# Kernel tuning notes

Measured on AMD Instinct MI355X. Metric: run time of the kernel, lower is better.

The kernel has to match this reference:

```python
import jax, jax.numpy as jnp
import numpy as np

# quantization / activation scales (stand-ins for act_scales dict entries)
S_IN = 0.05      # in_proj:input
S_Z = 0.02       # in_proj:output (also gate/z scale)
S_U = 0.01       # x_proj:input (conv output scale)
S_DTLN = 0.02    # dt_layernorm:output
S_B = 0.02       # B_layernorm:output
S_C = 0.02       # C_layernorm:output
S_DT = 0.01      # dt_proj:output
S_Y = 0.01       # out_proj:input
EPS = 1e-6
R = 128          # time_step_rank
N = 16           # ssm_state_size


def qa(x, s):
    # simulate int8 activation quantization (values kept in fp32)
    return jnp.clip(jnp.round(x / s), -128.0, 127.0)


def qw(w):
    # per-tensor symmetric int8 weight quantization
    s = jnp.max(jnp.abs(w)) / 127.0
    return jnp.clip(jnp.round(w / s), -128.0, 127.0), s


def rmsnorm_q(x, w, s):
    x = x.astype(jnp.float32)
    x = x * jax.lax.rsqrt(jnp.mean(x * x, axis=-1, keepdims=True) + EPS)
    return qa(w * x, s)


def ssm_scan(u, dt, A, Bm, Cm):
    # u, dt: [B, D, S]; Bm, Cm: [B, S, N]; A: [D, N]
    def step(h, xs):
        dt_t, u_t, B_t, C_t = xs                     # [B,D],[B,D],[B,N],[B,N]
        dA = jnp.exp(dt_t[..., None] * A)            # [B,D,N]
        h = h * dA + (dt_t * u_t)[..., None] * B_t[:, None, :]
        y = jnp.einsum('bdn,bn->bd', h, C_t)
        return h, y
    Bsz, Dd, S = u.shape
    h0 = jnp.zeros((Bsz, Dd, A.shape[1]), u.dtype)
    xs = (jnp.moveaxis(dt, 2, 0), jnp.moveaxis(u, 2, 0),
          jnp.moveaxis(Bm, 1, 0), jnp.moveaxis(Cm, 1, 0))
    _, ys = jax.lax.scan(step, h0, xs)               # ys: [S,B,D]
    return jnp.moveaxis(ys, 0, 2)                    # [B,D,S]


def setup_inputs() -> dict:
    key = jax.random.key(0)
    ks = jax.random.split(key, 10)
    B, S, H, Din, K = 2, 2048, 2048, 4096, 4
    return {
        'hidden_states': jax.random.normal(ks[0], (B, S, H), jnp.float32),
        'in_proj_w': jax.random.normal(ks[1], (2 * Din, H), jnp.float32) * 0.02,
        'conv_w': jax.random.normal(ks[2], (Din, K), jnp.float32) * 0.1,
        'conv_b': jax.random.normal(ks[3], (Din,), jnp.float32) * 0.01,
        'x_proj_w': jax.random.normal(ks[4], (R + 2 * N, Din), jnp.float32) * 0.02,
        'dt_ln_w': jnp.ones((R,), jnp.float32),
        'B_ln_w': jnp.ones((N,), jnp.float32),
        'C_ln_w': jnp.ones((N,), jnp.float32),
        'dt_proj_w': jax.random.normal(ks[5], (Din, R), jnp.float32) * 0.05,
        'dt_bias': jax.random.normal(ks[6], (Din,), jnp.float32) * 0.5 - 4.0,
        'A_log': jnp.log(jnp.broadcast_to(jnp.arange(1, N + 1, dtype=jnp.float32), (Din, N))),
        'D_skip': jnp.ones((Din,), jnp.float32),
        'out_proj_w': jax.random.normal(ks[7], (H, Din), jnp.float32) * 0.02,
    }


def reference(hidden_states, in_proj_w, conv_w, conv_b, x_proj_w, dt_ln_w,
              B_ln_w, C_ln_w, dt_proj_w, dt_bias, A_log, D_skip, out_proj_w):
    # --- in_proj (W8A8B8O8), then seqlen-last layout [B, 2D, S] ---
    x_q = qa(hidden_states, S_IN)
    wq, ws = qw(in_proj_w)
    proj_q = qa((x_q @ wq.T) * (S_IN * ws), S_Z)          # [B,S,2D] int8-valued
    proj_q = jnp.swapaxes(proj_q, 1, 2)                   # [B,2D,S]
    Din = proj_q.shape[1] // 2
    hs_q, gate_q = proj_q[:, :Din], proj_q[:, Din:]

    # --- quantized causal depthwise conv1d + silu (QCausalConv1D) ---
    cwq, cws = qw(conv_w)
    K = conv_w.shape[1]
    conv_out = jax.lax.conv_general_dilated(
        hs_q, cwq[:, None, :], (1,), [(K - 1, 0)],
        dimension_numbers=('NCH', 'OIH', 'NCH'), feature_group_count=Din)
    conv_out = conv_out * (S_Z * cws) + conv_b[None, :, None]
    u_q = qa(jax.nn.silu(conv_out), S_U)                  # [B,Din,S]

    # --- x_proj (W8A8BF16OF16) -> dt/B/C, inner RMSNorms + quant ---
    xwq, xws = qw(x_proj_w)
    ssm_p = (jnp.swapaxes(u_q, 1, 2) @ xwq.T) * (S_U * xws)   # [B,S,R+2N] float
    dt_q = rmsnorm_q(ssm_p[..., :R], dt_ln_w, S_DTLN)
    B_q = rmsnorm_q(ssm_p[..., R:R + N], B_ln_w, S_B)
    C_q = rmsnorm_q(ssm_p[..., R + N:], C_ln_w, S_C)

    # --- dt_proj (W8A8B8O8, bias folded into scan) ---
    dwq, dws = qw(dt_proj_w)
    dt8 = qa((dt_q @ dwq.T) * (S_DTLN * dws), S_DT)       # [B,S,Din]
    dt = jax.nn.softplus(jnp.swapaxes(dt8, 1, 2) * S_DT + dt_bias[None, :, None])

    # --- selective scan (QSScan): dequantize, recur, gate ---
    u = u_q * S_U
    A = -jnp.exp(A_log)
    ys = ssm_scan(u, dt, A, B_q * S_B, C_q * S_C)         # [B,Din,S]
    ys = ys + u * D_skip[None, :, None]
    ys = ys * jax.nn.silu(gate_q * S_Z)

    # --- QAct + out_proj (W8A8BF16OF16) ---
    y_q = qa(jnp.swapaxes(ys, 1, 2), S_Y)                 # [B,S,Din]
    owq, ows = qw(out_proj_w)
    return (y_q @ owq.T) * (S_Y * ows)                    # [B,S,H]
```

## Files before the change

### kernel.cpp

```cpp
#include <hip/hip_runtime.h>
#include <stdint.h>

typedef signed char i8;
typedef int v4i __attribute__((ext_vector_type(4)));

#define S_IN  0.05f
#define S_Z   0.02f
#define S_U   0.01f
#define S_DTLN 0.02f
#define S_B   0.02f
#define S_C   0.02f
#define S_DT  0.01f
#define S_Y   0.01f

__device__ __forceinline__ float q8f(float x, float s) {
    float r = rintf(x / s);
    return fmaxf(-128.0f, fminf(127.0f, r));
}
__device__ __forceinline__ int q8i(float x, float s) { return (int)q8f(x, s); }

__device__ __forceinline__ float softplus_f(float x) {
    return __fadd_rn(fmaxf(x, 0.0f), log1pf(expf(-fabsf(x))));
}

__device__ __forceinline__ int sbyte_of(int w, int j) {
    return (int)(signed char)((unsigned)w >> (j * 8));
}
__device__ __forceinline__ int ubyte_of(int w, int j) {
    return (int)(((unsigned)w >> (j * 8)) & 255u);
}

__device__ __forceinline__ void gload16(const i8* g, i8* lds) {
    __builtin_amdgcn_global_load_lds(
        (const __attribute__((address_space(1))) unsigned int*)g,
        (__attribute__((address_space(3))) unsigned int*)lds,
        16, 0, 0);
}

__global__ __launch_bounds__(256)
void k_maxabs(const float* __restrict__ w, long long n, unsigned* __restrict__ out) {
    unsigned m = 0;
    long long stride = (long long)gridDim.x * 256;
    for (long long i = (long long)blockIdx.x * 256 + threadIdx.x; i < n; i += stride)
        m = max(m, __float_as_uint(fabsf(w[i])));
    #pragma unroll
    for (int off = 32; off; off >>= 1) {
        unsigned o = (unsigned)__shfl_xor((int)m, off);
        m = max(m, o);
    }
    __shared__ unsigned sm[4];
    if ((threadIdx.x & 63) == 0) sm[threadIdx.x >> 6] = m;
    __syncthreads();
    if (threadIdx.x == 0) {
        unsigned r = max(max(sm[0], sm[1]), max(sm[2], sm[3]));
        atomicMax(out, r);
    }
}

__global__ __launch_bounds__(256)
void k_quant_w(const float* __restrict__ w, long long n,
               const unsigned* __restrict__ maxbits, i8* __restrict__ o) {
    long long i = ((long long)blockIdx.x * 256 + threadIdx.x) * 4;
    if (i >= n) return;
    float s = __uint_as_float(*maxbits) / 127.0f;
    float4 v = *(const float4*)(w + i);
    unsigned pk = ((unsigned)(q8i(v.x, s) & 255))
                | ((unsigned)(q8i(v.y, s) & 255) << 8)
                | ((unsigned)(q8i(v.z, s) & 255) << 16)
                | ((unsigned)(q8i(v.w, s) & 255) << 24);
    *(unsigned*)(o + i) = pk;
}

__global__ __launch_bounds__(256)
void k_quant_x(const float* __restrict__ x, long long n, float s, i8* __restrict__ o) {
    long long i = ((long long)blockIdx.x * 256 + threadIdx.x) * 4;
    if (i >= n) return;
    float4 v = *(const float4*)(x + i);
    unsigned pk = ((unsigned)(q8i(v.x, s) & 255))
                | ((unsigned)(q8i(v.y, s) & 255) << 8)
                | ((unsigned)(q8i(v.z, s) & 255) << 16)
                | ((unsigned)(q8i(v.w, s) & 255) << 24);
    *(unsigned*)(o + i) = pk;
}

template<int EPI>
__global__ __launch_bounds__(256)
void k_mgemm(const i8* __restrict__ A, const i8* __restrict__ Bw,
             int M, int N, int K,
             const unsigned* __restrict__ wmaxbits,
             void* __restrict__ out0, void* __restrict__ out1) {
    __shared__ i8 sA[16384];
    __shared__ i8 sB[16384];
    const int tid = threadIdx.x;
    const int w = tid >> 6;
    const int l = tid & 63;
    int id = blockIdx.y * gridDim.x + blockIdx.x;
    const int qq = (gridDim.x * gridDim.y) >> 3;
    id = (id & 7) * qq + (id >> 3);
    const int m0 = (id / gridDim.x) << 7;
    const int n0 = (id % gridDim.x) << 7;
    const int lr = l & 15;
    const int lk = l >> 4;
    const i8* gA = A  + (size_t)(m0 + lr) * K + lk * 16;
    const i8* gB = Bw + (size_t)(n0 + lr) * K + lk * 16;
    const size_t rowK16 = (size_t)16 * K;
    const int mw = (w >> 1) * 4;
    const int nw = (w & 1) * 4;
    const int rdoff = lk * 256 + lr * 16;
    v4i acc[4][4] = {};
    for (int k0 = 0; k0 < K; k0 += 128) {
        gload16(gA + rowK16 * w + k0,            sA + w * 2048);
        gload16(gA + rowK16 * w + k0 + 64,       sA + w * 2048 + 1024);
        gload16(gA + rowK16 * (4 + w) + k0,      sA + (4 + w) * 2048);
        gload16(gA + rowK16 * (4 + w) + k0 + 64, sA + (4 + w) * 2048 + 1024);
        gload16(gB + rowK16 * w + k0,            sB + w * 2048);
        gload16(gB + rowK16 * w + k0 + 64,       sB + w * 2048 + 1024);
        gload16(gB + rowK16 * (4 + w) + k0,      sB + (4 + w) * 2048);
        gload16(gB + rowK16 * (4 + w) + k0 + 64, sB + (4 + w) * 2048 + 1024);
        __syncthreads();
        #pragma unroll
        for (int k64 = 0; k64 < 2; k64++) {
            v4i af[4], bf[4];
            #pragma unroll
            for (int t = 0; t < 4; t++) {
                af[t] = *(const v4i*)(sA + (mw + t) * 2048 + k64 * 1024 + rdoff);
                bf[t] = *(const v4i*)(sB + (nw + t) * 2048 + k64 * 1024 + rdoff);
            }
            #pragma unroll
            for (int mt = 0; mt < 4; mt++)
                #pragma unroll
                for (int nt = 0; nt < 4; nt++)
                    acc[mt][nt] = __builtin_amdgcn_mfma_i32_16x16x64_i8(af[mt], bf[nt], acc[mt][nt], 0, 0, 0);
        }
        __syncthreads();
    }
    const float wsc = __uint_as_float(*wmaxbits) / 127.0f;
    const int m0w = m0 + (w >> 1) * 64;
    const int n0w = n0 + (w & 1) * 64;
    if constexpr (EPI == 0 || EPI == 2) {
        const float sc = (EPI == 0 ? S_IN : S_DTLN) * wsc;
        const float qs = (EPI == 0 ? S_Z : S_DT);
        const int b = m0w >> 11;
        #pragma unroll
        for (int nt = 0; nt < 4; nt++) {
            const int j = n0w + nt * 16 + lr;
            i8* dst;
            if constexpr (EPI == 0) dst = (j < 4096) ? (i8*)out0 : (i8*)out1;
            else dst = (i8*)out0;
            const int jj = j & 4095;
            #pragma unroll
            for (int mt = 0; mt < 4; mt++) {
                const int sbase = (m0w & 2047) + mt * 16 + lk * 4;
                unsigned pk = 0;
                #pragma unroll
                for (int r = 0; r < 4; r++) {
                    float v = (float)acc[mt][nt][r] * sc;
                    pk |= ((unsigned)(q8i(v, qs) & 255)) << (8 * r);
                }
                *(unsigned*)(dst + ((size_t)b * 4096 + jj) * 2048 + sbase) = pk;
            }
        }
    } else if constexpr (EPI == 1) {
        const float sc = S_U * wsc;
        float* O = (float*)out0;
        #pragma unroll
        for (int mt = 0; mt < 4; mt++)
            #pragma unroll
            for (int r = 0; r < 4; r++) {
                const int m = m0w + mt * 16 + lk * 4 + r;
                #pragma unroll
                for (int nt = 0; nt < 4; nt++) {
                    const int j = n0w + nt * 16 + lr;
                    if (j < 160)
                        O[(size_t)m * 160 + j] = (float)acc[mt][nt][r] * sc;
                }
            }
    } else {
        const float sc = S_Y * wsc;
        float* O = (float*)out0;
        #pragma unroll
        for (int mt = 0; mt < 4; mt++)
            #pragma unroll
            for (int r = 0; r < 4; r++) {
                const int m = m0w + mt * 16 + lk * 4 + r;
                #pragma unroll
                for (int nt = 0; nt < 4; nt++)
                    O[(size_t)m * N + n0w + nt * 16 + lr] = (float)acc[mt][nt][r] * sc;
            }
    }
}

__global__ __launch_bounds__(256)
void k_conv(const i8* __restrict__ hsq, const i8* __restrict__ cwq,
            const float* __restrict__ conv_b, const unsigned* __restrict__ cmaxbits,
            i8* __restrict__ uq, i8* __restrict__ uqT) {
    __shared__ char lt[64][68];
    const int tid = threadIdx.x;
    const int b = blockIdx.z;
    const int d0 = blockIdx.y << 6;
    const int s0 = blockIdx.x << 6;
    const int dl = tid >> 2;
    const int sg = tid & 3;
    const int d = d0 + dl;
    const int sbase = s0 + (sg << 4);
    const i8* xp = hsq + ((size_t)b * 4096 + d) * 2048;
    int v[19];
    #pragma unroll
    for (int i = 0; i < 19; i++) {
        int s = sbase - 3 + i;
        v[i] = (s >= 0) ? (int)xp[s] : 0;
    }
    const unsigned cw = *(const unsigned*)(cwq + (size_t)d * 4);
    const int w0 = (int)(char)(cw & 255);
    const int w1 = (int)(char)((cw >> 8) & 255);
    const int w2 = (int)(char)((cw >> 16) & 255);
    const int w3 = (int)(char)((cw >> 24) & 255);
    const float cws = __uint_as_float(*cmaxbits) / 127.0f;
    const float sc = S_Z * cws;
    const float bias = conv_b[d];
    unsigned pk[4] = {0, 0, 0, 0};
    #pragma unroll
    for (int t = 0; t < 16; t++) {
        int acc = v[t] * w0 + v[t + 1] * w1 + v[t + 2] * w2 + v[t + 3] * w3;
        float f = __fadd_rn(__fmul_rn((float)acc, sc), bias);
        float sig = 1.0f / (1.0f + expf(-f));
        float sl = __fmul_rn(f, sig);
        int q = q8i(sl, S_U);
        pk[t >> 2] |= ((unsigned)(q & 255)) << ((t & 3) * 8);
        lt[(sg << 4) + t][dl] = (char)q;
    }
    *(int4*)(uq + ((size_t)b * 4096 + d) * 2048 + sbase) = make_int4(pk[0], pk[1], pk[2], pk[3]);
    __syncthreads();
    const int rr = tid >> 2;
    const int wg = tid & 3;
    const int* rp = (const int*)(&lt[rr][wg << 4]);
    int4 o; o.x = rp[0]; o.y = rp[1]; o.z = rp[2]; o.w = rp[3];
    *(int4*)(uqT + ((size_t)b * 2048 + s0 + rr) * 4096 + d0 + (wg << 4)) = o;
}

__global__ __launch_bounds__(64)
void k_rms(const float* __restrict__ p,
           const float* __restrict__ wdt, const float* __restrict__ wB, const float* __restrict__ wC,
           i8* __restrict__ dtq, i8* __restrict__ bqT, i8* __restrict__ cqT) {
    const int row = blockIdx.x;
    const int lane = threadIdx.x;
    const float* x = p + (size_t)row * 160;
    float a0 = x[lane], a1 = x[64 + lane];
    float bb = (lane < 16) ? x[128 + lane] : 0.0f;
    float cc = (lane < 16) ? x[144 + lane] : 0.0f;
    float sdt = __fadd_rn(__fmul_rn(a0, a0), __fmul_rn(a1, a1));
    float sB = __fmul_rn(bb, bb);
    float sC = __fmul_rn(cc, cc);
    #pragma unroll
    for (int off = 32; off; off >>= 1) {
        sdt = __fadd_rn(sdt, __shfl_xor(sdt, off));
        sB  = __fadd_rn(sB,  __shfl_xor(sB, off));
        sC  = __fadd_rn(sC,  __shfl_xor(sC, off));
    }
    float rdt = 1.0f / sqrtf(sdt / 128.0f + 1e-6f);
    float rB  = 1.0f / sqrtf(sB / 16.0f + 1e-6f);
    float rC  = 1.0f / sqrtf(sC / 16.0f + 1e-6f);
    dtq[(size_t)row * 128 + lane]      = (i8)q8i(__fmul_rn(wdt[lane],      __fmul_rn(a0, rdt)), S_DTLN);
    dtq[(size_t)row * 128 + 64 + lane] = (i8)q8i(__fmul_rn(wdt[64 + lane], __fmul_rn(a1, rdt)), S_DTLN);
    if (lane < 16) {
        size_t tpos = ((size_t)(row >> 11) * 16 + lane) * 2048 + (row & 2047);
        bqT[tpos] = (i8)q8i(__fmul_rn(wB[lane], __fmul_rn(bb, rB)), S_B);
        cqT[tpos] = (i8)q8i(__fmul_rn(wC[lane], __fmul_rn(cc, rC)), S_C);
    }
}

__global__ __launch_bounds__(256)
void k_lut_dt(const float* __restrict__ dt_bias, float* __restrict__ lut) {
    const int d = blockIdx.x;
    const int q = threadIdx.x;
    const int sv = (q < 128) ? q : q - 256;
    const float bias = dt_bias[d];
    lut[(size_t)d * 256 + q] =
        softplus_f(__fadd_rn(__fmul_rn((float)sv, S_DT), bias));
}
__global__ __launch_bounds__(256)
void k_lut_silu(float* __restrict__ lut) {
    const int q = threadIdx.x;
    const int sv = (q < 128) ? q : q - 256;
    float gv = __fmul_rn((float)sv, S_Z);
    float sg = __fmul_rn(gv, 1.0f / (1.0f + expf(-gv)));
    lut[q] = sg;
}

__global__ __launch_bounds__(256)
void k_scan4(const i8* __restrict__ dt8, const i8* __restrict__ uq, const i8* __restrict__ gq,
             const i8* __restrict__ BqT, const i8* __restrict__ CqT,
             const float* __restrict__ lut_dt, const float* __restrict__ lut_silu,
             const float* __restrict__ A_log, const float* __restrict__ D_skip,
             i8* __restrict__ yq) {
    const int g = blockIdx.x * 256 + threadIdx.x;
    const int n = g & 15;
    const int bd = g >> 4;
    const int d = bd & 4095;
    const int b = bd >> 12;
    const float Acoef = -expf(A_log[(size_t)d * 16 + n]);
    const float Dd = D_skip[d];
    const float* ldt = lut_dt + (size_t)d * 256;
    const v4i* dtp = (const v4i*)(dt8 + (size_t)bd * 2048);
    const v4i* up  = (const v4i*)(uq  + (size_t)bd * 2048);
    const v4i* gp  = (const v4i*)(gq  + (size_t)bd * 2048);
    const v4i* Bp  = (const v4i*)(BqT + ((size_t)b * 16 + n) * 2048);
    const v4i* Cp  = (const v4i*)(CqT + ((size_t)b * 16 + n) * 2048);
    i8* yp = yq + (size_t)b * 2048 * 4096 + d;
    float h = 0.0f;
    v4i dtw = dtp[0], uw = up[0], gw = gp[0], bw = Bp[0], cw = Cp[0];
    for (int t = 0; t < 128; t++) {
        v4i ndt, nu, ng, nb, nc;
        if (t < 127) { ndt = dtp[t + 1]; nu = up[t + 1]; ng = gp[t + 1]; nb = Bp[t + 1]; nc = Cp[t + 1]; }
        float dtv[16], dA[16], pj[16], Cv[16], y[16];
        #pragma unroll
        for (int j = 0; j < 16; j++)
            dtv[j] = ldt[ubyte_of(dtw[j >> 2], j & 3)];
        #pragma unroll
        for (int j = 0; j < 16; j++)
            dA[j] = expf(__fmul_rn(dtv[j], Acoef));
        #pragma unroll
        for (int j = 0; j < 16; j++) {
            float uv = __fmul_rn((float)sbyte_of(uw[j >> 2], j & 3), S_U);
            float Bv = __fmul_rn((float)sbyte_of(bw[j >> 2], j & 3), S_B);
            Cv[j] = __fmul_rn((float)sbyte_of(cw[j >> 2], j & 3), S_C);
            pj[j] = __fmul_rn(__fmul_rn(dtv[j], uv), Bv);
        }
        #pragma unroll
        for (int j = 0; j < 16; j++) {
            h = __fadd_rn(__fmul_rn(h, dA[j]), pj[j]);
            y[j] = __fmul_rn(h, Cv[j]);
        }
        float w8[8];
        #pragma unroll
        for (int i = 0; i < 8; i++) {
            float a = y[2 * i], bq = y[2 * i + 1];
            float snd = (n & 1) ? a : bq;
            float rcv = __shfl_xor(snd, 1);
            float kept = (n & 1) ? bq : a;
            w8[i] = __fadd_rn(kept, rcv);
        }
        float w4[4];
        #pragma unroll
        for (int i = 0; i < 4; i++) {
            float a = w8[2 * i], bq = w8[2 * i + 1];
            float snd = (n & 2) ? a : bq;
            float rcv = __shfl_xor(snd, 2);
            float kept = (n & 2) ? bq : a;
            w4[i] = __fadd_rn(kept, rcv);
        }
        float w2[2];
        #pragma unroll
        for (int i = 0; i < 2; i++) {
            float a = w4[2 * i], bq = w4[2 * i + 1];
            float snd = (n & 4) ? a : bq;
            float rcv = __shfl_xor(snd, 4);
            float kept = (n & 4) ? bq : a;
            w2[i] = __fadd_rn(kept, rcv);
        }
        float ysave;
        {
            float a = w2[0], bq = w2[1];
            float snd = (n & 8) ? a : bq;
            float rcv = __shfl_xor(snd, 8);
            float kept = (n & 8) ? bq : a;
            ysave = __fadd_rn(kept, rcv);
        }
        int uws = (n & 8) ? ((n & 4) ? uw[3] : uw[2]) : ((n & 4) ? uw[1] : uw[0]);
        int gws = (n & 8) ? ((n & 4) ? gw[3] : gw[2]) : ((n & 4) ? gw[1] : gw[0]);
        float uvn = __fmul_rn((float)(int)(signed char)((unsigned)uws >> ((n & 3) * 8)), S_U);
        int gb = (int)(((unsigned)gws >> ((n & 3) * 8)) & 255u);
        float ys = __fadd_rn(ysave, __fmul_rn(uvn, Dd));
        float sg = lut_silu[gb];
        float vv = __fmul_rn(ys, sg);
        yp[(size_t)(t * 16 + n) * 4096] = (i8)q8i(vv, S_Y);
        if (t < 127) { dtw = ndt; uw = nu; gw = ng; bw = nb; cw = nc; }
    }
}

extern "C" void kernel_launch(void* const* d_in, const int* in_sizes, int n_in,
                              void* d_out, int out_size, void* d_ws, size_t ws_size,
                              hipStream_t stream) {
    const float* hidden   = (const float*)d_in[0];
    const float* in_proj  = (const float*)d_in[1];
    const float* conv_w   = (const float*)d_in[2];
    const float* conv_b   = (const float*)d_in[3];
    const float* x_proj   = (const float*)d_in[4];
    const float* dt_ln    = (const float*)d_in[5];
    const float* B_ln     = (const float*)d_in[6];
    const float* C_ln     = (const float*)d_in[7];
    const float* dt_proj  = (const float*)d_in[8];
    const float* dt_bias  = (const float*)d_in[9];
    const float* A_log    = (const float*)d_in[10];
    const float* D_skip   = (const float*)d_in[11];
    const float* out_proj = (const float*)d_in[12];
    float* out = (float*)d_out;

    char* ws = (char*)d_ws;
    unsigned* scales = (unsigned*)ws;
    i8* WQ   = (i8*)(ws + 256);
    i8* XQ   = (i8*)(ws + 16777472);
    i8* HSQ  = (i8*)(ws + 25166080);
    char* S0 = ws + 41943296;
    float* SSMP = (float*)S0;
    i8* XWQp = (i8*)(S0 + 2621440);
    i8* DTQb = (i8*)(S0 + 3670016);
    i8* DWQ  = (i8*)(S0 + 4194304);
    i8* CWQ  = (i8*)(S0 + 4718592);
    float* LUTSI = (float*)(S0 + 4734976);
    i8* BQT  = (i8*)(S0 + 4736000);
    i8* CQT  = (i8*)(S0 + 4801536);
    float* LUTDT = (float*)S0;

    i8* GQ = (i8*)d_out;
    i8* UQ = (i8*)d_out + 16777216;
    i8* UQT = WQ;
    i8* OWQ = XQ;
    i8* DT8 = HSQ;
    i8* YQ  = WQ;

    hipMemsetAsync(scales, 0, 256, stream);
    hipMemsetAsync(XWQp, 0, 1048576, stream);

    k_maxabs<<<2048, 256, 0, stream>>>(in_proj, 16777216LL, scales + 0);
    k_maxabs<<<64,   256, 0, stream>>>(conv_w,  16384LL,    scales + 1);
    k_maxabs<<<512,  256, 0, stream>>>(x_proj,  655360LL,   scales + 2);
    k_maxabs<<<512,  256, 0, stream>>>(dt_proj, 524288LL,   scales + 3);
    k_maxabs<<<1024, 256, 0, stream>>>(out_proj, 8388608LL, scales + 4);

    k_quant_w<<<16384, 256, 0, stream>>>(in_proj, 16777216LL, scales + 0, WQ);
    k_quant_w<<<16,    256, 0, stream>>>(conv_w,  16384LL,    scales + 1, CWQ);
    k_quant_w<<<640,   256, 0, stream>>>(x_proj,  655360LL,   scales + 2, XWQp);
    k_quant_w<<<512,   256, 0, stream>>>(dt_proj, 524288LL,   scales + 3, DWQ);
    k_quant_x<<<8192,  256, 0, stream>>>(hidden,  8388608LL,  S_IN, XQ);

    k_mgemm<0><<<dim3(64, 32), 256, 0, stream>>>(XQ, WQ, 4096, 8192, 2048, scales + 0, HSQ, GQ);

    k_quant_w<<<8192, 256, 0, stream>>>(out_proj, 8388608LL, scales + 4, OWQ);

    dim3 gc(32, 64, 2);
    k_conv<<<gc, 256, 0, stream>>>(HSQ, CWQ, conv_b, scales + 1, UQ, UQT);

    k_mgemm<1><<<dim3(2, 32), 256, 0, stream>>>(UQT, XWQp, 4096, 256, 4096, scales + 2, SSMP, nullptr);

    k_rms<<<4096, 64, 0, stream>>>(SSMP, dt_ln, B_ln, C_ln, DTQb, BQT, CQT);

    k_mgemm<2><<<dim3(32, 32), 256, 0, stream>>>(DTQb, DWQ, 4096, 4096, 128, scales + 3, DT8, nullptr);

    k_lut_dt<<<4096, 256, 0, stream>>>(dt_bias, LUTDT);
    k_lut_silu<<<1, 256, 0, stream>>>(LUTSI);

    k_scan4<<<512, 256, 0, stream>>>(DT8, UQ, GQ, BQT, CQT, LUTDT, LUTSI, A_log, D_skip, YQ);

    k_mgemm<3><<<dim3(16, 32), 256, 0, stream>>>(YQ, OWQ, 4096, 2048, 4096, scales + 4, out, nullptr);
}
```

Measured before the change: 702.0 us.

## Split-K the x_proj GEMM with int atomics and merge small prep kernels

The x_proj GEMM (grid 2x32, K=4096) now splits K across 8 z-slices. Each slice atomically adds its int32 partial sums into a zeroed buffer, and k_rms applies the dequant scale when it reads them. The many per-tensor maxabs and quantize launches, and the two LUT kernels, are each folded into a single launch that dispatches by block index. The goal is to fill the GPU on the undersized GEMM and cut launch overhead, at the cost of an extra memset and atomic traffic.

```diff
diff --git a/kernel.cpp b/kernel.cpp
--- a/kernel.cpp
+++ b/kernel.cpp
@@ -38,10 +38,19 @@
 }
 
 __global__ __launch_bounds__(256)
-void k_maxabs(const float* __restrict__ w, long long n, unsigned* __restrict__ out) {
+void k_maxabs_all(const float* __restrict__ a0, const float* __restrict__ a1,
+                  const float* __restrict__ a2, const float* __restrict__ a3,
+                  const float* __restrict__ a4, unsigned* __restrict__ out) {
+    int bid = blockIdx.x;
+    const float* w; long long n; int slot, nb;
+    if (bid < 2048)      { w = a0; n = 16777216LL; slot = 0; nb = 2048; }
+    else if (bid < 2112) { w = a1; n = 16384LL;    slot = 1; nb = 64;   bid -= 2048; }
+    else if (bid < 2624) { w = a2; n = 655360LL;   slot = 2; nb = 512;  bid -= 2112; }
+    else if (bid < 3136) { w = a3; n = 524288LL;   slot = 3; nb = 512;  bid -= 2624; }
+    else                 { w = a4; n = 8388608LL;  slot = 4; nb = 1024; bid -= 3136; }
     unsigned m = 0;
-    long long stride = (long long)gridDim.x * 256;
-    for (long long i = (long long)blockIdx.x * 256 + threadIdx.x; i < n; i += stride)
+    long long stride = (long long)nb * 256;
+    for (long long i = (long long)bid * 256 + threadIdx.x; i < n; i += stride)
         m = max(m, __float_as_uint(fabsf(w[i])));
     #pragma unroll
     for (int off = 32; off; off >>= 1) {
@@ -53,8 +62,30 @@
     __syncthreads();
     if (threadIdx.x == 0) {
         unsigned r = max(max(sm[0], sm[1]), max(sm[2], sm[3]));
-        atomicMax(out, r);
-    }
+        atomicMax(out + slot, r);
+    }
+}
+
+__global__ __launch_bounds__(256)
+void k_quant_all(const float* __restrict__ a0, const float* __restrict__ a1,
+                 const float* __restrict__ a2, const float* __restrict__ a3,
+                 const float* __restrict__ ax, const unsigned* __restrict__ scales,
+                 i8* __restrict__ o0, i8* __restrict__ o1, i8* __restrict__ o2,
+                 i8* __restrict__ o3, i8* __restrict__ ox) {
+    int bid = blockIdx.x;
+    const float* w; i8* o; float s;
+    if (bid < 16384)      { w = a0; o = o0; s = __uint_as_float(scales[0]) / 127.0f; }
+    else if (bid < 16400) { w = a1; o = o1; s = __uint_as_float(scales[1]) / 127.0f; bid -= 16384; }
+    else if (bid < 17040) { w = a2; o = o2; s = __uint_as_float(scales[2]) / 127.0f; bid -= 16400; }
+    else if (bid < 17552) { w = a3; o = o3; s = __uint_as_float(scales[3]) / 127.0f; bid -= 17040; }
+    else                  { w = ax; o = ox; s = S_IN;                                 bid -= 17552; }
+    long long i = ((long long)bid * 256 + threadIdx.x) * 4;
+    float4 v = *(const float4*)(w + i);
+    unsigned pk = ((unsigned)(q8i(v.x, s) & 255))
+                | ((unsigned)(q8i(v.y, s) & 255) << 8)
+                | ((unsigned)(q8i(v.z, s) & 255) << 16)
+                | ((unsigned)(q8i(v.w, s) & 255) << 24);
+    *(unsigned*)(o + i) = pk;
 }
 
 __global__ __launch_bounds__(256)
@@ -64,18 +95,6 @@
     if (i >= n) return;
     float s = __uint_as_float(*maxbits) / 127.0f;
     float4 v = *(const float4*)(w + i);
-    unsigned pk = ((unsigned)(q8i(v.x, s) & 255))
-                | ((unsigned)(q8i(v.y, s) & 255) << 8)
-                | ((unsigned)(q8i(v.z, s) & 255) << 16)
-                | ((unsigned)(q8i(v.w, s) & 255) << 24);
-    *(unsigned*)(o + i) = pk;
-}
-
-__global__ __launch_bounds__(256)
-void k_quant_x(const float* __restrict__ x, long long n, float s, i8* __restrict__ o) {
-    long long i = ((long long)blockIdx.x * 256 + threadIdx.x) * 4;
-    if (i >= n) return;
-    float4 v = *(const float4*)(x + i);
     unsigned pk = ((unsigned)(q8i(v.x, s) & 255))
                 | ((unsigned)(q8i(v.y, s) & 255) << 8)
                 | ((unsigned)(q8i(v.z, s) & 255) << 16)
@@ -99,6 +118,8 @@
     id = (id & 7) * qq + (id >> 3);
     const int m0 = (id / gridDim.x) << 7;
     const int n0 = (id % gridDim.x) << 7;
+    const int kLen = K / gridDim.z;
+    const int kOff = blockIdx.z * kLen;
     const int lr = l & 15;
     const int lk = l >> 4;
     const i8* gA = A  + (size_t)(m0 + lr) * K + lk * 16;
@@ -108,7 +129,7 @@
     const int nw = (w & 1) * 4;
     const int rdoff = lk * 256 + lr * 16;
     v4i acc[4][4] = {};
-    for (int k0 = 0; k0 < K; k0 += 128) {
+    for (int k0 = kOff; k0 < kOff + kLen; k0 += 128) {
         gload16(gA + rowK16 * w + k0,            sA + w * 2048);
         gload16(gA + rowK16 * w + k0 + 64,       sA + w * 2048 + 1024);
         gload16(gA + rowK16 * (4 + w) + k0,      sA + (4 + w) * 2048);
@@ -161,8 +182,7 @@
             }
         }
     } else if constexpr (EPI == 1) {
-        const float sc = S_U * wsc;
-        float* O = (float*)out0;
+        int* O = (int*)out0;
         #pragma unroll
         for (int mt = 0; mt < 4; mt++)
             #pragma unroll
@@ -172,7 +192,7 @@
                 for (int nt = 0; nt < 4; nt++) {
                     const int j = n0w + nt * 16 + lr;
                     if (j < 160)
-                        O[(size_t)m * 160 + j] = (float)acc[mt][nt][r] * sc;
+                        atomicAdd(O + (size_t)m * 160 + j, acc[mt][nt][r]);
                 }
             }
     } else {
@@ -239,15 +259,17 @@
 }
 
 __global__ __launch_bounds__(64)
-void k_rms(const float* __restrict__ p,
+void k_rms(const int* __restrict__ p, const unsigned* __restrict__ xsc,
            const float* __restrict__ wdt, const float* __restrict__ wB, const float* __restrict__ wC,
            i8* __restrict__ dtq, i8* __restrict__ bqT, i8* __restrict__ cqT) {
     const int row = blockIdx.x;
     const int lane = threadIdx.x;
-    const float* x = p + (size_t)row * 160;
-    float a0 = x[lane], a1 = x[64 + lane];
-    float bb = (lane < 16) ? x[128 + lane] : 0.0f;
-    float cc = (lane < 16) ? x[144 + lane] : 0.0f;
+    const float scp = S_U * (__uint_as_float(*xsc) / 127.0f);
+    const int* x = p + (size_t)row * 160;
+    float a0 = (float)x[lane] * scp;
+    float a1 = (float)x[64 + lane] * scp;
+    float bb = (lane < 16) ? (float)x[128 + lane] * scp : 0.0f;
+    float cc = (lane < 16) ? (float)x[144 + lane] * scp : 0.0f;
     float sdt = __fadd_rn(__fmul_rn(a0, a0), __fmul_rn(a1, a1));
     float sB = __fmul_rn(bb, bb);
     float sC = __fmul_rn(cc, cc);
@@ -270,21 +292,20 @@
 }
 
 __global__ __launch_bounds__(256)
-void k_lut_dt(const float* __restrict__ dt_bias, float* __restrict__ lut) {
-    const int d = blockIdx.x;
+void k_lut_all(const float* __restrict__ dt_bias, float* __restrict__ lutdt,
+               float* __restrict__ lutsi) {
     const int q = threadIdx.x;
     const int sv = (q < 128) ? q : q - 256;
-    const float bias = dt_bias[d];
-    lut[(size_t)d * 256 + q] =
-        softplus_f(__fadd_rn(__fmul_rn((float)sv, S_DT), bias));
-}
-__global__ __launch_bounds__(256)
-void k_lut_silu(float* __restrict__ lut) {
-    const int q = threadIdx.x;
-    const int sv = (q < 128) ? q : q - 256;
-    float gv = __fmul_rn((float)sv, S_Z);
-    float sg = __fmul_rn(gv, 1.0f / (1.0f + expf(-gv)));
-    lut[q] = sg;
+    if (blockIdx.x < 4096) {
+        const int d = blockIdx.x;
+        const float bias = dt_bias[d];
+        lutdt[(size_t)d * 256 + q] =
+            softplus_f(__fadd_rn(__fmul_rn((float)sv, S_DT), bias));
+    } else {
+        float gv = __fmul_rn((float)sv, S_Z);
+        float sg = __fmul_rn(gv, 1.0f / (1.0f + expf(-gv)));
+        lutsi[q] = sg;
+    }
 }
 
 __global__ __launch_bounds__(256)
@@ -402,7 +423,7 @@
     i8* XQ   = (i8*)(ws + 16777472);
     i8* HSQ  = (i8*)(ws + 25166080);
     char* S0 = ws + 41943296;
-    float* SSMP = (float*)S0;
+    int*  SSMP = (int*)S0;
     i8* XWQp = (i8*)(S0 + 2621440);
     i8* DTQb = (i8*)(S0 + 3670016);
     i8* DWQ  = (i8*)(S0 + 4194304);
@@ -420,19 +441,13 @@
     i8* YQ  = WQ;
 
     hipMemsetAsync(scales, 0, 256, stream);
+    hipMemsetAsync(SSMP, 0, 2621440, stream);
     hipMemsetAsync(XWQp, 0, 1048576, stream);
 
-    k_maxabs<<<2048, 256, 0, stream>>>(in_proj, 16777216LL, scales + 0);
-    k_maxabs<<<64,   256, 0, stream>>>(conv_w,  16384LL,    scales + 1);
-    k_maxabs<<<512,  256, 0, stream>>>(x_proj,  655360LL,   scales + 2);
-    k_maxabs<<<512,  256, 0, stream>>>(dt_proj, 524288LL,   scales + 3);
-    k_maxabs<<<1024, 256, 0, stream>>>(out_proj, 8388608LL, scales + 4);
-
-    k_quant_w<<<16384, 256, 0, stream>>>(in_proj, 16777216LL, scales + 0, WQ);
-    k_quant_w<<<16,    256, 0, stream>>>(conv_w,  16384LL,    scales + 1, CWQ);
-    k_quant_w<<<640,   256, 0, stream>>>(x_proj,  655360LL,   scales + 2, XWQp);
-    k_quant_w<<<512,   256, 0, stream>>>(dt_proj, 524288LL,   scales + 3, DWQ);
-    k_quant_x<<<8192,  256, 0, stream>>>(hidden,  8388608LL,  S_IN, XQ);
+    k_maxabs_all<<<4160, 256, 0, stream>>>(in_proj, conv_w, x_proj, dt_proj, out_proj, scales);
+
+    k_quant_all<<<25744, 256, 0, stream>>>(in_proj, conv_w, x_proj, dt_proj, hidden,
+                                           scales, WQ, CWQ, XWQp, DWQ, XQ);
 
     k_mgemm<0><<<dim3(64, 32), 256, 0, stream>>>(XQ, WQ, 4096, 8192, 2048, scales + 0, HSQ, GQ);
 
@@ -441,14 +456,13 @@
     dim3 gc(32, 64, 2);
     k_conv<<<gc, 256, 0, stream>>>(HSQ, CWQ, conv_b, scales + 1, UQ, UQT);
 
-    k_mgemm<1><<<dim3(2, 32), 256, 0, stream>>>(UQT, XWQp, 4096, 256, 4096, scales + 2, SSMP, nullptr);
-
-    k_rms<<<4096, 64, 0, stream>>>(SSMP, dt_ln, B_ln, C_ln, DTQb, BQT, CQT);
+    k_mgemm<1><<<dim3(2, 32, 8), 256, 0, stream>>>(UQT, XWQp, 4096, 256, 4096, scales + 2, SSMP, nullptr);
+
+    k_rms<<<4096, 64, 0, stream>>>(SSMP, scales + 2, dt_ln, B_ln, C_ln, DTQb, BQT, CQT);
 
     k_mgemm<2><<<dim3(32, 32), 256, 0, stream>>>(DTQb, DWQ, 4096, 4096, 128, scales + 3, DT8, nullptr);
 
-    k_lut_dt<<<4096, 256, 0, stream>>>(dt_bias, LUTDT);
-    k_lut_silu<<<1, 256, 0, stream>>>(LUTSI);
+    k_lut_all<<<4097, 256, 0, stream>>>(dt_bias, LUTDT, LUTSI);
 
     k_scan4<<<512, 256, 0, stream>>>(DT8, UQ, GQ, BQT, CQT, LUTDT, LUTSI, A_log, D_skip, YQ);
 
```

Measured after the change: 658.3 us. 1.07x faster.
